# Kernel optimization log

Measured on AMD Instinct MI355X. Metric: run time of the kernel, lower is better.

The kernel has to match this reference:

```python
import jax, jax.numpy as jnp
import numpy as np

B, L, D, V, M = 8, 64, 256, 4096, 16


def _norm(a):
    # torch .std(-1) uses ddof=1 (unbiased)
    return a / (1e-5 + jnp.std(a, axis=-1, keepdims=True, ddof=1))


def setup_inputs() -> dict:
    key = jax.random.key(0)
    ks = jax.random.split(key, 13)
    s = 0.05
    return {
        "x": jax.random.randint(ks[0], (B, L), 0, V),
        "z": jax.random.randint(ks[1], (B, L), 0, V),
        "embed_w": jax.random.normal(ks[2], (V, D), dtype=jnp.float32) * s,
        "init_w": jax.random.normal(ks[3], (D, M), dtype=jnp.float32) * s,
        "trans_w": jax.random.normal(ks[4], (D, D), dtype=jnp.float32) * s,
        "trans_b": jax.random.normal(ks[5], (D,), dtype=jnp.float32) * s,
        "core_w": jax.random.normal(ks[6], (D, D), dtype=jnp.float32) * s,
        "upd_w": jax.random.normal(ks[7], (D, D), dtype=jnp.float32) * s,
        "xks_w": jax.random.normal(ks[8], (2, D), dtype=jnp.float32) * s,
        "xkd_w": jax.random.normal(ks[9], (D, D), dtype=jnp.float32) * s,
        "xkd_b": jax.random.normal(ks[10], (D,), dtype=jnp.float32) * s,
        "emi_w": jax.random.normal(ks[11], (D, D), dtype=jnp.float32) * s,
        "emi_b": jax.random.normal(ks[12], (D,), dtype=jnp.float32) * s,
    }


def reference(x, z, embed_w, init_w, trans_w, trans_b, core_w, upd_w,
              xks_w, xkd_w, xkd_b, emi_w, emi_b):
    # loss() sets y = x * 0 (all-zero token ids)
    ze = _norm(embed_w[z])                      # (B, L, D)
    ye = _norm(embed_w[x * 0])                  # (B, L, D)
    Bq, Lq, Dq = ze.shape

    # init_state.weight.T[None, 0:1] -> column 0, broadcast to (B, L, D), then norm
    xsa0 = _norm(jnp.broadcast_to(init_w[:, 0][None, None, :], (Bq, Lq, Dq)))

    def step(xsa, _):
        xnew = (jnp.roll(xsa, 1, axis=1) @ trans_w
                + jnp.roll(xsa, -1, axis=1) @ trans_w.T
                + xsa @ core_w
                + ze @ upd_w.T
                + trans_b) / 3.0
        return xnew, None

    xsa, _ = jax.lax.scan(step, xsa0, None, length=Lq)

    # mixture head
    xkey_static = jnp.broadcast_to(xks_w[None], (Bq, 2, Dq))          # (B, 2, D)
    xkey_dynamic = ye @ xkd_w.T + xkd_b                                # (B, L, D)
    xkey = jnp.concatenate([xkey_static, xkey_dynamic], axis=1)       # (B, 2+L, D)

    emit = xsa @ emi_w.T + emi_b                                       # (B, L, D)
    cand = jnp.concatenate(
        [emit[:, :, None], ze[:, :, None],
         jnp.broadcast_to(ye[:, None], (Bq, Lq, Lq, Dq))], axis=2)     # (B, L, 2+L, D)

    sel = jax.nn.log_softmax(jnp.einsum('bld,bkd->blk', xsa, xkey), axis=-1)  # (B, L, 2+L)
    lptok_c = jax.nn.log_softmax(cand @ embed_w.T, axis=-1)            # (B, L, 2+L, V)
    lptok = jax.nn.logsumexp(sel[..., None] + lptok_c, axis=-2)        # (B, L, V)
    lptok = jnp.exp(lptok / 2.0)

    cent = jnp.take_along_axis(lptok, x[:, :, None], axis=-1)[..., 0]  # (B, L)
    return -cent.mean(-1)                                              # (B,)
```

## Files before the change

### kernel.cpp

```cpp
#include <hip/hip_runtime.h>
#include <hip/hip_bf16.h>
#include <math.h>

#define BB 8
#define LL 64
#define DD 256
#define VV 4096
#define RR 512
#define K3 768

typedef __attribute__((ext_vector_type(4))) float f32x4;
typedef __attribute__((ext_vector_type(8))) short bf16x8;
typedef __attribute__((ext_vector_type(4))) unsigned short u16x4;
typedef unsigned long long u64;

#define WS_ZE      0
#define WS_ZEU3    (WS_ZE + RR*DD)
#define WS_WCT     (WS_ZEU3 + RR*DD)
#define WS_XSA0    (WS_WCT + DD*K3)
#define WS_XSA1    (WS_XSA0 + RR*DD)
#define WS_EMIT    (WS_XSA1 + RR*DD)
#define WS_YVEC    (WS_EMIT + RR*DD)
#define WS_X0VEC   (WS_YVEC + DD)
#define WS_YK      (WS_X0VEC + DD)
#define WS_YLOG    (WS_YK + DD)
#define WS_YLSE    (WS_YLOG + VV)
#define WS_SEL     (WS_YLSE + 8)
#define WS_TOKS    WS_SEL
#define WS_HPART   WS_WCT
#define WS_TWT     WS_XSA0
#define WS_CWT     (WS_XSA0 + 65536)
#define WS_EHI     861184
#define WS_ELO     (WS_EHI + VV*DD/2)

__device__ __forceinline__ float waveSum(float v) {
#pragma unroll
  for (int o = 32; o > 0; o >>= 1) v += __shfl_xor(v, o, 64);
  return v;
}

__device__ __forceinline__ float blockSum256(float v) {
  __shared__ float red[4];
  int lane = threadIdx.x & 63, w = threadIdx.x >> 6;
  v = waveSum(v);
  __syncthreads();
  if (lane == 0) red[w] = v;
  __syncthreads();
  return red[0] + red[1] + red[2] + red[3];
}

__device__ __forceinline__ unsigned short f2bf(float f) {
  unsigned int u = __float_as_uint(f);
  unsigned int r = (u + 0x7fffu + ((u >> 16) & 1u)) >> 16;
  return (unsigned short)r;
}
__device__ __forceinline__ float bf2f(unsigned short h) {
  return __uint_as_float(((unsigned int)h) << 16);
}

union U64F2 { u64 u; float f[2]; };

__global__ __launch_bounds__(256) void k_norm_rows(
    const int* __restrict__ z, const float* __restrict__ embed,
    const float* __restrict__ initw, float* __restrict__ ws) {
  int r = blockIdx.x, d = threadIdx.x;
  float a; float* dst;
  if (r < RR) { int tok = z[r]; a = embed[tok * DD + d]; dst = ws + WS_ZE + r * DD; }
  else if (r == RR) { a = embed[d]; dst = ws + WS_YVEC; }
  else { a = initw[d * 16]; dst = ws + WS_X0VEC; }
  float s  = blockSum256(a);
  float sq = blockSum256(a * a);
  float mean = s * (1.0f / DD);
  float var = fmaxf((sq - (float)DD * mean * mean) * (1.0f / (DD - 1)), 0.0f);
  dst[d] = a / (1e-5f + sqrtf(var));
}

__global__ __launch_bounds__(256) void k_rowmat2(
    const float* __restrict__ in, const float* __restrict__ W,
    const float* __restrict__ bias, float* __restrict__ out, float scale) {
  int r0 = blockIdx.x * 2, d = threadIdx.x;
  __shared__ float u[2][260];
  u[0][d] = in[r0 * DD + d];
  u[1][d] = in[(r0 + 1) * DD + d];
  __syncthreads();
  float a0 = 0.f, a1 = 0.f;
  const float4* w4 = (const float4*)(W + d * DD);
  const float4* u0 = (const float4*)&u[0][0];
  const float4* u1 = (const float4*)&u[1][0];
#pragma unroll 8
  for (int k4 = 0; k4 < 64; k4++) {
    float4 w = w4[k4], x0 = u0[k4], x1 = u1[k4];
    a0 += x0.x*w.x + x0.y*w.y + x0.z*w.z + x0.w*w.w;
    a1 += x1.x*w.x + x1.y*w.y + x1.z*w.z + x1.w*w.w;
  }
  float b = bias[d];
  out[r0 * DD + d]       = (a0 + b) * scale;
  out[(r0 + 1) * DD + d] = (a1 + b) * scale;
}

__global__ __launch_bounds__(256) void k_tr2(
    const float* __restrict__ tw, const float* __restrict__ cw,
    float* __restrict__ ws) {
  int c = blockIdx.x, k = threadIdx.x;
  ws[WS_TWT + c * DD + k] = tw[k * DD + c];
  ws[WS_CWT + c * DD + k] = cw[k * DD + c];
}

__global__ __launch_bounds__(256) void k_zmat2(
    const float* __restrict__ tw, float* __restrict__ ws) {
  int r0 = blockIdx.x * 2, c = threadIdx.x;
  int b = r0 >> 6, l = r0 & 63;
  const float* zb = ws + WS_ZEU3 + (size_t)b * 64 * DD;
  float* zout = ws + WS_XSA1;
  __shared__ float zs[4][260];
#pragma unroll
  for (int j = 0; j < 4; ++j) {
    int ll = (l + j - 1 + 64) & 63;
    zs[j][c] = zb[ll * DD + c];
  }
  __syncthreads();
  const float4* wA = (const float4*)(ws + WS_TWT + (size_t)c * DD);
  const float4* wB = (const float4*)(tw + (size_t)c * DD);
  const float4* wC = (const float4*)(ws + WS_CWT + (size_t)c * DD);
  const float4* zm0 = (const float4*)&zs[0][0];
  const float4* z00 = (const float4*)&zs[1][0];
  const float4* zp0 = (const float4*)&zs[2][0];
  const float4* zp1 = (const float4*)&zs[3][0];
  float a0 = 0.f, a1 = 0.f;
#pragma unroll 8
  for (int k4 = 0; k4 < 64; ++k4) {
    float4 A4 = wA[k4], B4 = wB[k4], C4 = wC[k4];
    float4 m0 = zm0[k4], z0 = z00[k4], p0 = zp0[k4], p1 = zp1[k4];
    a0 += m0.x*A4.x + m0.y*A4.y + m0.z*A4.z + m0.w*A4.w
        + p0.x*B4.x + p0.y*B4.y + p0.z*B4.z + p0.w*B4.w
        + z0.x*C4.x + z0.y*C4.y + z0.z*C4.z + z0.w*C4.w;
    a1 += z0.x*A4.x + z0.y*A4.y + z0.z*A4.z + z0.w*A4.w
        + p1.x*B4.x + p1.y*B4.y + p1.z*B4.z + p1.w*B4.w
        + p0.x*C4.x + p0.y*C4.y + p0.z*C4.z + p0.w*C4.w;
  }
  const float inv3 = 1.0f / 3.0f;
  zout[(size_t)r0 * DD + c]       = a0 * inv3 + zs[1][c];
  zout[(size_t)(r0 + 1) * DD + c] = a1 * inv3 + zs[2][c];
}

__global__ __launch_bounds__(256) void k_build_w2(
    const float* __restrict__ tw, const float* __restrict__ cw,
    float* __restrict__ ws) {
  int k = blockIdx.x, c = threadIdx.x;
  const float* twT = ws + WS_TWT;
  __shared__ float rA[DD], rB[DD], rC[DD];
  const float inv9 = 1.0f / 9.0f;
  rA[c] = tw[k * DD + c] * inv9;
  rB[c] = twT[k * DD + c] * inv9;
  rC[c] = cw[k * DD + c] * inv9;
  __syncthreads();
  float a2 = 0.f, m1 = 0.f, m0 = 0.f, m3 = 0.f, b2 = 0.f;
#pragma unroll 4
  for (int j = 0; j < DD; ++j) {
    float Aj = tw[j * DD + c];
    float Bj = twT[j * DD + c];
    float Cj = cw[j * DD + c];
    float ra = rA[j], rb = rB[j], rc = rC[j];
    a2 += ra * Aj;
    m1 += rc * Aj + ra * Cj;
    m0 += rb * Aj + ra * Bj + rc * Cj;
    m3 += rc * Bj + rb * Cj;
    b2 += rb * Bj;
  }
  float* p0 = ws + WS_WCT;
  float* p3 = ws + WS_ZEU3;
  p0[k * DD + c]               = a2;
  p0[65536 + k * DD + c]       = m1;
  p0[2 * 65536 + k * DD + c]   = m0;
  p3[k * DD + c]               = m3;
  p3[65536 + k * DD + c]       = b2;
}

__global__ __launch_bounds__(256) void k_split_e(
    const float* __restrict__ e, unsigned short* __restrict__ eh,
    unsigned short* __restrict__ el) {
  int i = (blockIdx.x * 256 + threadIdx.x) * 4;
  float4 v = *(const float4*)(e + i);
  float f[4] = {v.x, v.y, v.z, v.w};
  u16x4 h, l;
#pragma unroll
  for (int j = 0; j < 4; ++j) {
    unsigned short hb = f2bf(f[j]);
    h[j] = hb;
    l[j] = f2bf(f[j] - bf2f(hb));
  }
  *(u16x4*)(eh + i) = h;
  *(u16x4*)(el + i) = l;
}

__global__ __launch_bounds__(256) void k_ylog(
    const float* __restrict__ embed, float* __restrict__ ws) {
  __shared__ float y[DD];
  int t = threadIdx.x;
  y[t] = ws[WS_YVEC + t];
  __syncthreads();
  int w = t >> 6, lane = t & 63;
  for (int i = 0; i < 16; i++) {
    int v = blockIdx.x * 64 + i * 4 + w;
    float p = 0.f;
#pragma unroll
    for (int j = 0; j < 4; j++) p += y[lane + 64*j] * embed[v * DD + lane + 64*j];
    p = waveSum(p);
    if (lane == 0) ws[WS_YLOG + v] = p;
  }
}

__global__ void k_zero_cnt(int* __restrict__ c) {
  c[blockIdx.x * 256 + threadIdx.x] = 0;
}

__global__ __launch_bounds__(256, 2) void k_scan(float* __restrict__ ws) {
  const int bid = blockIdx.x;
  const int rg = bid & 63, cg = bid >> 6;
  const int b = rg >> 3, rgl = rg & 7, l0 = rgl * 8;
  const int t = threadIdx.x, lane = t & 63;
  const int cl = t & 7, rs = t >> 3;
  const int c0 = cg * 32 + cl * 4;

  __shared__ float S[12 * 264];
  __shared__ float PAR[32 * 260];
  __shared__ float PAR2[4 * 256];
  __shared__ float ZB[256];

  int* tok = (int*)(ws + WS_TOKS);

  const float* Wp[5] = {ws + WS_WCT, ws + WS_WCT + 65536, ws + WS_WCT + 2*65536,
                        ws + WS_ZEU3, ws + WS_ZEU3 + 65536};
  f32x4 wreg[40];
#pragma unroll
  for (int p = 0; p < 5; ++p)
#pragma unroll
    for (int q = 0; q < 2; ++q)
#pragma unroll
      for (int kk = 0; kk < 4; ++kk)
        wreg[p * 8 + q * 4 + kk] =
            *(const f32x4*)&Wp[p][(size_t)(rs * 8 + q * 4 + kk) * DD + c0];

  {
    int r = t >> 5, c = t & 31;
    ZB[r * 32 + c] = ws[WS_XSA1 + (size_t)(b * 64 + l0 + r) * DD + cg * 32 + c];
  }

  const int nb0 = b * 8 + ((rgl + 7) & 7);
  const int nb1 = b * 8 + rgl;
  const int nb2 = b * 8 + ((rgl + 1) & 7);
  const int myl = (lane == 0) ? nb0 : (lane == 1) ? nb1 : nb2;

  for (int st = 0; st < 32; ++st) {
    const float* xin  = ws + ((st & 1) ? WS_XSA1 : WS_XSA0);
    float*       xout = ws + ((st & 1) ? WS_XSA0 : WS_XSA1);

    if (st > 0) {
      const int tg = st << 3;
      while (true) {
        int v = __hip_atomic_load(tok + myl * 32, __ATOMIC_RELAXED,
                                  __HIP_MEMORY_SCOPE_AGENT);
        if (__all(v >= tg)) break;
        __builtin_amdgcn_s_sleep(1);
      }
    }

#pragma unroll
    for (int it = 0; it < 6; ++it) {
      int idx = it * 256 + t;
      int j = idx >> 7;
      int kk = (idx & 127) << 1;
      const u64* src = (st == 0)
          ? (const u64*)(ws + WS_X0VEC + kk)
          : (const u64*)(xin + (size_t)(b * 64 + ((l0 + j - 2 + 64) & 63)) * DD + kk);
      u64 v = __hip_atomic_load(src, __ATOMIC_RELAXED, __HIP_MEMORY_SCOPE_AGENT);
      *(u64*)(&S[j * 264 + kk]) = v;
    }
    __syncthreads();

    f32x4 acc[8];
#pragma unroll
    for (int r = 0; r < 8; ++r) acc[r] = (f32x4){0.f, 0.f, 0.f, 0.f};

#pragma unroll
    for (int p = 0; p < 5; ++p) {
#pragma unroll
      for (int r = 0; r < 8; ++r) {
        int j = r + p;
#pragma unroll
        for (int q = 0; q < 2; ++q) {
          f32x4 xv = *(const f32x4*)&S[j * 264 + rs * 8 + q * 4];
          acc[r] += xv.x * wreg[p * 8 + q * 4 + 0];
          acc[r] += xv.y * wreg[p * 8 + q * 4 + 1];
          acc[r] += xv.z * wreg[p * 8 + q * 4 + 2];
          acc[r] += xv.w * wreg[p * 8 + q * 4 + 3];
        }
      }
    }

#pragma unroll
    for (int r = 0; r < 8; ++r)
      *(f32x4*)&PAR[rs * 260 + r * 32 + cl * 4] = acc[r];
    __syncthreads();

    {
      int u = t & 63, v = t >> 6;
      f32x4 s4 = (f32x4){0.f, 0.f, 0.f, 0.f};
#pragma unroll
      for (int i = 0; i < 8; ++i)
        s4 += *(const f32x4*)&PAR[(v * 8 + i) * 260 + u * 4];
      *(f32x4*)&PAR2[v * 256 + u * 4] = s4;
    }
    __syncthreads();

    if (t < 64) {
      int r = t >> 3, c8 = t & 7;
      f32x4 s4 = (f32x4){0.f, 0.f, 0.f, 0.f};
#pragma unroll
      for (int v = 0; v < 4; ++v)
        s4 += *(const f32x4*)&PAR2[v * 256 + t * 4];
      f32x4 zb = *(const f32x4*)&ZB[r * 32 + c8 * 4];
      s4 += zb;
      size_t off = (size_t)(b * 64 + l0 + r) * DD + cg * 32 + c8 * 4;
      U64F2 lo, hi;
      lo.f[0] = s4.x; lo.f[1] = s4.y;
      hi.f[0] = s4.z; hi.f[1] = s4.w;
      __hip_atomic_store((u64*)(xout + off),     lo.u, __ATOMIC_RELAXED, __HIP_MEMORY_SCOPE_AGENT);
      __hip_atomic_store((u64*)(xout + off + 2), hi.u, __ATOMIC_RELAXED, __HIP_MEMORY_SCOPE_AGENT);
    }

    __syncthreads();
    if (t == 0)
      __hip_atomic_fetch_add(tok + nb1 * 32, 1, __ATOMIC_RELAXED,
                             __HIP_MEMORY_SCOPE_AGENT);
  }
}

__global__ __launch_bounds__(256) void k_head_mfma(
    const float* __restrict__ uemit, const float* __restrict__ uze,
    const unsigned short* __restrict__ eh, const unsigned short* __restrict__ el,
    float* __restrict__ hpart) {
  int row0 = blockIdx.x * 32;
  int v0 = blockIdx.y * 128;
  int t = threadIdx.x, lane = t & 63, w = t >> 6;
  int wr = w >> 1, wc = w & 1;
  __shared__ unsigned short UH[32 * 264];
  __shared__ unsigned short UL[32 * 264];
  const float* src = (row0 < RR) ? (uemit + (size_t)row0 * DD)
                                 : (uze + (size_t)(row0 - RR) * DD);
#pragma unroll
  for (int it = 0; it < 4; ++it) {
    int r = it * 8 + (t >> 5);
    int c8 = (t & 31) * 8;
    float4 a = *(const float4*)(src + (size_t)r * DD + c8);
    float4 b2 = *(const float4*)(src + (size_t)r * DD + c8 + 4);
    float fa[8] = {a.x, a.y, a.z, a.w, b2.x, b2.y, b2.z, b2.w};
    u16x4 h0, l0v, h1, l1;
#pragma unroll
    for (int j = 0; j < 4; ++j) {
      unsigned short hb = f2bf(fa[j]);
      h0[j] = hb; l0v[j] = f2bf(fa[j] - bf2f(hb));
      unsigned short hb1 = f2bf(fa[4 + j]);
      h1[j] = hb1; l1[j] = f2bf(fa[4 + j] - bf2f(hb1));
    }
    *(u16x4*)(&UH[r * 264 + c8])     = h0;
    *(u16x4*)(&UH[r * 264 + c8 + 4]) = h1;
    *(u16x4*)(&UL[r * 264 + c8])     = l0v;
    *(u16x4*)(&UL[r * 264 + c8 + 4]) = l1;
  }
  __syncthreads();

  f32x4 acc[4];
#pragma unroll
  for (int q = 0; q < 4; ++q) acc[q] = (f32x4){0.f, 0.f, 0.f, 0.f};

  int arow = wr * 16 + (lane & 15);
  int kof = 8 * (lane >> 4);
  const unsigned short* Ah = &UH[arow * 264 + kof];
  const unsigned short* Al = &UL[arow * 264 + kof];
  int vbase = v0 + wc * 64 + (lane & 15);

#pragma unroll
  for (int p = 0; p < 3; ++p) {
    const unsigned short* Ab = (p == 2) ? Al : Ah;
    const unsigned short* Ebl = ((p == 1) ? el : eh) + (size_t)vbase * DD + kof;
#pragma unroll
    for (int ks = 0; ks < 8; ++ks) {
      int k0 = ks * 32;
      bf16x8 a = *(const bf16x8*)(Ab + k0);
#pragma unroll
      for (int vt = 0; vt < 4; ++vt) {
        bf16x8 bfr = *(const bf16x8*)(Ebl + vt * 16 * DD + k0);
        acc[vt] = __builtin_amdgcn_mfma_f32_16x16x32_bf16(a, bfr, acc[vt], 0, 0, 0);
      }
    }
  }

  int chunk = blockIdx.y * 2 + wc;
#pragma unroll
  for (int i = 0; i < 4; ++i) {
    float mm = -1e30f;
#pragma unroll
    for (int vt = 0; vt < 4; ++vt) mm = fmaxf(mm, acc[vt][i]);
#pragma unroll
    for (int o = 1; o < 16; o <<= 1) mm = fmaxf(mm, __shfl_xor(mm, o, 64));
    float ss = 0.f;
#pragma unroll
    for (int vt = 0; vt < 4; ++vt) ss += __expf(acc[vt][i] - mm);
#pragma unroll
    for (int o = 1; o < 16; o <<= 1) ss += __shfl_xor(ss, o, 64);
    if ((lane & 15) == 0) {
      int row = row0 + wr * 16 + (lane >> 4) * 4 + i;
      hpart[(row * 64 + chunk) * 2]     = mm;
      hpart[(row * 64 + chunk) * 2 + 1] = ss;
    }
  }
}

__global__ __launch_bounds__(256) void k_finish(
    const int* __restrict__ x, const float* __restrict__ embed,
    const float* __restrict__ xks, const float* __restrict__ xkdw,
    const float* __restrict__ xkdb, float* __restrict__ ws,
    float* __restrict__ out) {
  int b = blockIdx.x, t = threadIdx.x, lane = t & 63, w = t >> 6;
  __shared__ float YK[DD];
  __shared__ float rm[4], rv[4];
  __shared__ float ylse_s;
  __shared__ float sel0[64], sel1[64], sel2[64], tg0[64], tg1[64];
  __shared__ float ls0s[64], ls1s[64];

  {
    float acc = xkdb[t];
    const float4* yv4 = (const float4*)(ws + WS_YVEC);
    const float4* w4 = (const float4*)(xkdw + (size_t)t * DD);
    float a = 0.f;
#pragma unroll 8
    for (int k4 = 0; k4 < 64; ++k4) {
      float4 yv = yv4[k4], wv = w4[k4];
      a += yv.x*wv.x + yv.y*wv.y + yv.z*wv.z + yv.w*wv.w;
    }
    YK[t] = acc + a;
  }
  {
    float m = -1e30f, s = 0.f;
    for (int v = t; v < VV; v += 256) {
      float lg = ws[WS_YLOG + v];
      float mn = fmaxf(m, lg);
      s = s * __expf(m - mn) + __expf(lg - mn);
      m = mn;
    }
#pragma unroll
    for (int o = 32; o > 0; o >>= 1) {
      float mo = __shfl_xor(m, o, 64), so = __shfl_xor(s, o, 64);
      float mn = fmaxf(m, mo);
      s = s * __expf(m - mn) + so * __expf(mo - mn);
      m = mn;
    }
    if (lane == 0) { rm[w] = m; rv[w] = s; }
  }
  __syncthreads();
  if (t == 0) {
    float M = fmaxf(fmaxf(rm[0], rm[1]), fmaxf(rm[2], rm[3]));
    float S = rv[0]*__expf(rm[0]-M) + rv[1]*__expf(rm[1]-M) +
              rv[2]*__expf(rm[2]-M) + rv[3]*__expf(rm[3]-M);
    ylse_s = M + logf(S);
  }

  const float* hp = ws + WS_HPART;
  for (int i = 0; i < 16; ++i) {
    int l = w * 16 + i, r = b * 64 + l;
    float4 xs = *(const float4*)&ws[WS_XSA0 + (size_t)r * DD + lane * 4];
    float4 k0 = *(const float4*)&xks[lane * 4];
    float4 k1 = *(const float4*)&xks[DD + lane * 4];
    float4 yk4 = *(const float4*)&YK[lane * 4];
    float s0 = waveSum(xs.x*k0.x + xs.y*k0.y + xs.z*k0.z + xs.w*k0.w);
    float s1 = waveSum(xs.x*k1.x + xs.y*k1.y + xs.z*k1.z + xs.w*k1.w);
    float s2 = waveSum(xs.x*yk4.x + xs.y*yk4.y + xs.z*yk4.z + xs.w*yk4.w);
    int xv = x[r];
    float4 e4 = *(const float4*)&embed[(size_t)xv * DD + lane * 4];
    float4 em = *(const float4*)&ws[WS_EMIT + (size_t)r * DD + lane * 4];
    float4 zr = *(const float4*)&ws[WS_ZE + (size_t)r * DD + lane * 4];
    float t0 = waveSum(em.x*e4.x + em.y*e4.y + em.z*e4.z + em.w*e4.w);
    float t1 = waveSum(zr.x*e4.x + zr.y*e4.y + zr.z*e4.z + zr.w*e4.w);
    float m0 = hp[((size_t)r * 64 + lane) * 2];
    float q0 = hp[((size_t)r * 64 + lane) * 2 + 1];
    float m1 = hp[((size_t)(RR + r) * 64 + lane) * 2];
    float q1 = hp[((size_t)(RR + r) * 64 + lane) * 2 + 1];
#pragma unroll
    for (int o = 32; o > 0; o >>= 1) {
      float mo = __shfl_xor(m0, o, 64), so = __shfl_xor(q0, o, 64);
      float mn = fmaxf(m0, mo);
      q0 = q0 * __expf(m0 - mn) + so * __expf(mo - mn);
      m0 = mn;
      mo = __shfl_xor(m1, o, 64); so = __shfl_xor(q1, o, 64);
      mn = fmaxf(m1, mo);
      q1 = q1 * __expf(m1 - mn) + so * __expf(mo - mn);
      m1 = mn;
    }
    if (lane == 0) {
      sel0[l] = s0; sel1[l] = s1; sel2[l] = s2;
      tg0[l] = t0; tg1[l] = t1;
      ls0s[l] = m0 + logf(q0);
      ls1s[l] = m1 + logf(q1);
    }
  }
  __syncthreads();
  if (w == 0) {
    int l = lane, r = b * 64 + l;
    float s0 = sel0[l], s1 = sel1[l], s2 = sel2[l];
    float mx = fmaxf(s0, fmaxf(s1, s2));
    float den = expf(s0 - mx) + expf(s1 - mx) + 64.f * expf(s2 - mx);
    float lsel = mx + logf(den);
    int xv = x[r];
    float P0 = expf(s0 - lsel + tg0[l] - ls0s[l]);
    float P1 = expf(s1 - lsel + tg1[l] - ls1s[l]);
    float Py = expf(s2 - lsel + ws[WS_YLOG + xv] - ylse_s);
    float cent = sqrtf(P0 + P1 + 64.f * Py);
    float sum = waveSum(cent);
    if (lane == 0) out[b] = -(sum * (1.0f / 64.f));
  }
}

extern "C" void kernel_launch(void* const* d_in, const int* in_sizes, int n_in,
                              void* d_out, int out_size, void* d_ws, size_t ws_size,
                              hipStream_t stream) {
  (void)in_sizes; (void)n_in; (void)out_size; (void)ws_size;
  const int*   x     = (const int*)d_in[0];
  const int*   z     = (const int*)d_in[1];
  const float* embed = (const float*)d_in[2];
  const float* initw = (const float*)d_in[3];
  const float* tw    = (const float*)d_in[4];
  const float* tb    = (const float*)d_in[5];
  const float* cw    = (const float*)d_in[6];
  const float* uw    = (const float*)d_in[7];
  const float* xks   = (const float*)d_in[8];
  const float* xkdw  = (const float*)d_in[9];
  const float* xkdb  = (const float*)d_in[10];
  const float* emiw  = (const float*)d_in[11];
  const float* emib  = (const float*)d_in[12];
  float* ws  = (float*)d_ws;
  float* out = (float*)d_out;

  hipLaunchKernelGGL(k_norm_rows, dim3(RR + 2), dim3(256), 0, stream, z, embed, initw, ws);
  hipLaunchKernelGGL(k_rowmat2,   dim3(256),    dim3(256), 0, stream,
                     ws + WS_ZE, uw, tb, ws + WS_ZEU3, 1.0f / 3.0f);
  hipLaunchKernelGGL(k_tr2,       dim3(256),    dim3(256), 0, stream, tw, cw, ws);
  hipLaunchKernelGGL(k_zmat2,     dim3(256),    dim3(256), 0, stream, tw, ws);
  hipLaunchKernelGGL(k_build_w2,  dim3(256),    dim3(256), 0, stream, tw, cw, ws);
  hipLaunchKernelGGL(k_split_e,   dim3(1024),   dim3(256), 0, stream, embed,
                     (unsigned short*)(ws + WS_EHI), (unsigned short*)(ws + WS_ELO));
  hipLaunchKernelGGL(k_ylog,      dim3(64),     dim3(256), 0, stream, embed, ws);

  hipLaunchKernelGGL(k_zero_cnt, dim3(8), dim3(256), 0, stream, (int*)(ws + WS_TOKS));
  hipLaunchKernelGGL(k_scan, dim3(512), dim3(256), 0, stream, ws);

  hipLaunchKernelGGL(k_rowmat2, dim3(256), dim3(256), 0, stream,
                     ws + WS_XSA0, emiw, emib, ws + WS_EMIT, 1.0f);
  hipLaunchKernelGGL(k_head_mfma, dim3(32, 32), dim3(256), 0, stream,
                     ws + WS_EMIT, ws + WS_ZE,
                     (const unsigned short*)(ws + WS_EHI),
                     (const unsigned short*)(ws + WS_ELO),
                     ws + WS_HPART);
  hipLaunchKernelGGL(k_finish, dim3(8), dim3(256), 0, stream,
                     x, embed, xks, xkdw, xkdb, ws, out);
}
```

Measured before the change: 368.0 us.

## Merge prep kernels and fold embed split, ylog and emit matmul into scan

Folds the ten small launches into four. The transpose goes into the norm kernel, zmat and build_w run as one grid with the counter reset added, and the bf16 embed split, ylog and emit projection are appended to the scan kernel as extra blocks or an epilogue. The aim is to cut launch overhead and let independent work fill idle CUs while the persistent scan runs. The risk is that extra blocks in the scan grid could be scheduled ahead of scan blocks that spin-wait, and the added epilogue wait lengthens the scan blocks.

```diff
diff --git a/kernel.cpp b/kernel.cpp
--- a/kernel.cpp
+++ b/kernel.cpp
@@ -39,16 +39,6 @@
   return v;
 }
 
-__device__ __forceinline__ float blockSum256(float v) {
-  __shared__ float red[4];
-  int lane = threadIdx.x & 63, w = threadIdx.x >> 6;
-  v = waveSum(v);
-  __syncthreads();
-  if (lane == 0) red[w] = v;
-  __syncthreads();
-  return red[0] + red[1] + red[2] + red[3];
-}
-
 __device__ __forceinline__ unsigned short f2bf(float f) {
   unsigned int u = __float_as_uint(f);
   unsigned int r = (u + 0x7fffu + ((u >> 16) & 1u)) >> 16;
@@ -60,19 +50,36 @@
 
 union U64F2 { u64 u; float f[2]; };
 
-__global__ __launch_bounds__(256) void k_norm_rows(
+__global__ __launch_bounds__(256) void k_prep1(
     const int* __restrict__ z, const float* __restrict__ embed,
-    const float* __restrict__ initw, float* __restrict__ ws) {
-  int r = blockIdx.x, d = threadIdx.x;
-  float a; float* dst;
-  if (r < RR) { int tok = z[r]; a = embed[tok * DD + d]; dst = ws + WS_ZE + r * DD; }
-  else if (r == RR) { a = embed[d]; dst = ws + WS_YVEC; }
-  else { a = initw[d * 16]; dst = ws + WS_X0VEC; }
-  float s  = blockSum256(a);
-  float sq = blockSum256(a * a);
-  float mean = s * (1.0f / DD);
-  float var = fmaxf((sq - (float)DD * mean * mean) * (1.0f / (DD - 1)), 0.0f);
-  dst[d] = a / (1e-5f + sqrtf(var));
+    const float* __restrict__ initw, const float* __restrict__ tw,
+    const float* __restrict__ cw, float* __restrict__ ws) {
+  int bid = blockIdx.x, d = threadIdx.x;
+  __shared__ float red[4];
+  if (bid < RR + 2) {
+    float a; float* dst;
+    if (bid < RR) { int tok = z[bid]; a = embed[tok * DD + d]; dst = ws + WS_ZE + bid * DD; }
+    else if (bid == RR) { a = embed[d]; dst = ws + WS_YVEC; }
+    else { a = initw[d * 16]; dst = ws + WS_X0VEC; }
+    int lane = d & 63, w = d >> 6;
+    float s = waveSum(a);
+    __syncthreads();
+    if (lane == 0) red[w] = s;
+    __syncthreads();
+    float sum = red[0] + red[1] + red[2] + red[3];
+    float sq = waveSum(a * a);
+    __syncthreads();
+    if (lane == 0) red[w] = sq;
+    __syncthreads();
+    float sqs = red[0] + red[1] + red[2] + red[3];
+    float mean = sum * (1.0f / DD);
+    float var = fmaxf((sqs - (float)DD * mean * mean) * (1.0f / (DD - 1)), 0.0f);
+    dst[d] = a / (1e-5f + sqrtf(var));
+  } else {
+    int c = bid - (RR + 2);
+    ws[WS_TWT + c * DD + d] = tw[d * DD + c];
+    ws[WS_CWT + c * DD + d] = cw[d * DD + c];
+  }
 }
 
 __global__ __launch_bounds__(256) void k_rowmat2(
@@ -98,134 +105,129 @@
   out[(r0 + 1) * DD + d] = (a1 + b) * scale;
 }
 
-__global__ __launch_bounds__(256) void k_tr2(
+__global__ __launch_bounds__(256) void k_prep3(
     const float* __restrict__ tw, const float* __restrict__ cw,
     float* __restrict__ ws) {
-  int c = blockIdx.x, k = threadIdx.x;
-  ws[WS_TWT + c * DD + k] = tw[k * DD + c];
-  ws[WS_CWT + c * DD + k] = cw[k * DD + c];
-}
-
-__global__ __launch_bounds__(256) void k_zmat2(
-    const float* __restrict__ tw, float* __restrict__ ws) {
-  int r0 = blockIdx.x * 2, c = threadIdx.x;
-  int b = r0 >> 6, l = r0 & 63;
-  const float* zb = ws + WS_ZEU3 + (size_t)b * 64 * DD;
-  float* zout = ws + WS_XSA1;
+  int bid = blockIdx.x, c = threadIdx.x;
   __shared__ float zs[4][260];
-#pragma unroll
-  for (int j = 0; j < 4; ++j) {
-    int ll = (l + j - 1 + 64) & 63;
-    zs[j][c] = zb[ll * DD + c];
-  }
-  __syncthreads();
-  const float4* wA = (const float4*)(ws + WS_TWT + (size_t)c * DD);
-  const float4* wB = (const float4*)(tw + (size_t)c * DD);
-  const float4* wC = (const float4*)(ws + WS_CWT + (size_t)c * DD);
-  const float4* zm0 = (const float4*)&zs[0][0];
-  const float4* z00 = (const float4*)&zs[1][0];
-  const float4* zp0 = (const float4*)&zs[2][0];
-  const float4* zp1 = (const float4*)&zs[3][0];
-  float a0 = 0.f, a1 = 0.f;
+  __shared__ float rA[DD], rB[DD], rC[DD];
+  if (bid < 256) {
+    int r0 = bid * 2;
+    int b = r0 >> 6, l = r0 & 63;
+    const float* zb = ws + WS_ZEU3 + (size_t)b * 64 * DD;
+    float* zout = ws + WS_XSA1;
+#pragma unroll
+    for (int j = 0; j < 4; ++j) {
+      int ll = (l + j - 1 + 64) & 63;
+      zs[j][c] = zb[ll * DD + c];
+    }
+    __syncthreads();
+    const float4* wA = (const float4*)(ws + WS_TWT + (size_t)c * DD);
+    const float4* wB = (const float4*)(tw + (size_t)c * DD);
+    const float4* wC = (const float4*)(ws + WS_CWT + (size_t)c * DD);
+    const float4* zm0 = (const float4*)&zs[0][0];
+    const float4* z00 = (const float4*)&zs[1][0];
+    const float4* zp0 = (const float4*)&zs[2][0];
+    const float4* zp1 = (const float4*)&zs[3][0];
+    float a0 = 0.f, a1 = 0.f;
 #pragma unroll 8
-  for (int k4 = 0; k4 < 64; ++k4) {
-    float4 A4 = wA[k4], B4 = wB[k4], C4 = wC[k4];
-    float4 m0 = zm0[k4], z0 = z00[k4], p0 = zp0[k4], p1 = zp1[k4];
-    a0 += m0.x*A4.x + m0.y*A4.y + m0.z*A4.z + m0.w*A4.w
-        + p0.x*B4.x + p0.y*B4.y + p0.z*B4.z + p0.w*B4.w
-        + z0.x*C4.x + z0.y*C4.y + z0.z*C4.z + z0.w*C4.w;
-    a1 += z0.x*A4.x + z0.y*A4.y + z0.z*A4.z + z0.w*A4.w
-        + p1.x*B4.x + p1.y*B4.y + p1.z*B4.z + p1.w*B4.w
-        + p0.x*C4.x + p0.y*C4.y + p0.z*C4.z + p0.w*C4.w;
-  }
-  const float inv3 = 1.0f / 3.0f;
-  zout[(size_t)r0 * DD + c]       = a0 * inv3 + zs[1][c];
-  zout[(size_t)(r0 + 1) * DD + c] = a1 * inv3 + zs[2][c];
-}
-
-__global__ __launch_bounds__(256) void k_build_w2(
-    const float* __restrict__ tw, const float* __restrict__ cw,
-    float* __restrict__ ws) {
-  int k = blockIdx.x, c = threadIdx.x;
-  const float* twT = ws + WS_TWT;
-  __shared__ float rA[DD], rB[DD], rC[DD];
-  const float inv9 = 1.0f / 9.0f;
-  rA[c] = tw[k * DD + c] * inv9;
-  rB[c] = twT[k * DD + c] * inv9;
-  rC[c] = cw[k * DD + c] * inv9;
-  __syncthreads();
-  float a2 = 0.f, m1 = 0.f, m0 = 0.f, m3 = 0.f, b2 = 0.f;
+    for (int k4 = 0; k4 < 64; ++k4) {
+      float4 A4 = wA[k4], B4 = wB[k4], C4 = wC[k4];
+      float4 m0 = zm0[k4], z0 = z00[k4], p0 = zp0[k4], p1 = zp1[k4];
+      a0 += m0.x*A4.x + m0.y*A4.y + m0.z*A4.z + m0.w*A4.w
+          + p0.x*B4.x + p0.y*B4.y + p0.z*B4.z + p0.w*B4.w
+          + z0.x*C4.x + z0.y*C4.y + z0.z*C4.z + z0.w*C4.w;
+      a1 += z0.x*A4.x + z0.y*A4.y + z0.z*A4.z + z0.w*A4.w
+          + p1.x*B4.x + p1.y*B4.y + p1.z*B4.z + p1.w*B4.w
+          + p0.x*C4.x + p0.y*C4.y + p0.z*C4.z + p0.w*C4.w;
+    }
+    const float inv3 = 1.0f / 3.0f;
+    zout[(size_t)r0 * DD + c]       = a0 * inv3 + zs[1][c];
+    zout[(size_t)(r0 + 1) * DD + c] = a1 * inv3 + zs[2][c];
+  } else if (bid < 512) {
+    int k = bid - 256;
+    const float* twT = ws + WS_TWT;
+    const float inv9 = 1.0f / 9.0f;
+    rA[c] = tw[k * DD + c] * inv9;
+    rB[c] = twT[k * DD + c] * inv9;
+    rC[c] = cw[k * DD + c] * inv9;
+    __syncthreads();
+    float a2 = 0.f, m1 = 0.f, m0 = 0.f, m3 = 0.f, b2 = 0.f;
 #pragma unroll 4
-  for (int j = 0; j < DD; ++j) {
-    float Aj = tw[j * DD + c];
-    float Bj = twT[j * DD + c];
-    float Cj = cw[j * DD + c];
-    float ra = rA[j], rb = rB[j], rc = rC[j];
-    a2 += ra * Aj;
-    m1 += rc * Aj + ra * Cj;
-    m0 += rb * Aj + ra * Bj + rc * Cj;
-    m3 += rc * Bj + rb * Cj;
-    b2 += rb * Bj;
-  }
-  float* p0 = ws + WS_WCT;
-  float* p3 = ws + WS_ZEU3;
-  p0[k * DD + c]               = a2;
-  p0[65536 + k * DD + c]       = m1;
-  p0[2 * 65536 + k * DD + c]   = m0;
-  p3[k * DD + c]               = m3;
-  p3[65536 + k * DD + c]       = b2;
-}
-
-__global__ __launch_bounds__(256) void k_split_e(
-    const float* __restrict__ e, unsigned short* __restrict__ eh,
-    unsigned short* __restrict__ el) {
-  int i = (blockIdx.x * 256 + threadIdx.x) * 4;
-  float4 v = *(const float4*)(e + i);
-  float f[4] = {v.x, v.y, v.z, v.w};
-  u16x4 h, l;
-#pragma unroll
-  for (int j = 0; j < 4; ++j) {
-    unsigned short hb = f2bf(f[j]);
-    h[j] = hb;
-    l[j] = f2bf(f[j] - bf2f(hb));
-  }
-  *(u16x4*)(eh + i) = h;
-  *(u16x4*)(el + i) = l;
-}
-
-__global__ __launch_bounds__(256) void k_ylog(
-    const float* __restrict__ embed, float* __restrict__ ws) {
-  __shared__ float y[DD];
-  int t = threadIdx.x;
-  y[t] = ws[WS_YVEC + t];
-  __syncthreads();
-  int w = t >> 6, lane = t & 63;
-  for (int i = 0; i < 16; i++) {
-    int v = blockIdx.x * 64 + i * 4 + w;
-    float p = 0.f;
-#pragma unroll
-    for (int j = 0; j < 4; j++) p += y[lane + 64*j] * embed[v * DD + lane + 64*j];
-    p = waveSum(p);
-    if (lane == 0) ws[WS_YLOG + v] = p;
-  }
-}
-
-__global__ void k_zero_cnt(int* __restrict__ c) {
-  c[blockIdx.x * 256 + threadIdx.x] = 0;
-}
-
-__global__ __launch_bounds__(256, 2) void k_scan(float* __restrict__ ws) {
+    for (int j = 0; j < DD; ++j) {
+      float Aj = tw[j * DD + c];
+      float Bj = twT[j * DD + c];
+      float Cj = cw[j * DD + c];
+      float ra = rA[j], rb = rB[j], rc = rC[j];
+      a2 += ra * Aj;
+      m1 += rc * Aj + ra * Cj;
+      m0 += rb * Aj + ra * Bj + rc * Cj;
+      m3 += rc * Bj + rb * Cj;
+      b2 += rb * Bj;
+    }
+    float* p0 = ws + WS_WCT;
+    float* p3 = ws + WS_ZEU3;
+    p0[k * DD + c]               = a2;
+    p0[65536 + k * DD + c]       = m1;
+    p0[2 * 65536 + k * DD + c]   = m0;
+    p3[k * DD + c]               = m3;
+    p3[65536 + k * DD + c]       = b2;
+  } else {
+    ((int*)(ws + WS_TOKS))[(bid - 512) * 256 + c] = 0;
+  }
+}
+
+__global__ __launch_bounds__(256, 2) void k_scan_big(
+    float* __restrict__ ws, const float* __restrict__ embed,
+    const float* __restrict__ emiw, const float* __restrict__ emib) {
   const int bid = blockIdx.x;
-  const int rg = bid & 63, cg = bid >> 6;
-  const int b = rg >> 3, rgl = rg & 7, l0 = rgl * 8;
   const int t = threadIdx.x, lane = t & 63;
-  const int cl = t & 7, rs = t >> 3;
-  const int c0 = cg * 32 + cl * 4;
 
   __shared__ float S[12 * 264];
   __shared__ float PAR[32 * 260];
   __shared__ float PAR2[4 * 256];
   __shared__ float ZB[256];
+
+  if (bid >= 512) {
+    int eb = bid - 512;
+    if (eb < 1024) {
+      unsigned short* eh = (unsigned short*)(ws + WS_EHI);
+      unsigned short* el = (unsigned short*)(ws + WS_ELO);
+      int i = (eb * 256 + t) * 4;
+      float4 v = *(const float4*)(embed + i);
+      float f[4] = {v.x, v.y, v.z, v.w};
+      u16x4 h, l;
+#pragma unroll
+      for (int j = 0; j < 4; ++j) {
+        unsigned short hb = f2bf(f[j]);
+        h[j] = hb;
+        l[j] = f2bf(f[j] - bf2f(hb));
+      }
+      *(u16x4*)(eh + i) = h;
+      *(u16x4*)(el + i) = l;
+    } else {
+      int yb = eb - 1024;
+      float* y = S;
+      y[t] = ws[WS_YVEC + t];
+      __syncthreads();
+      int w = t >> 6;
+      for (int i = 0; i < 16; i++) {
+        int v = yb * 64 + i * 4 + w;
+        float p = 0.f;
+#pragma unroll
+        for (int j = 0; j < 4; j++)
+          p += y[lane + 64*j] * embed[(size_t)v * DD + lane + 64*j];
+        p = waveSum(p);
+        if (lane == 0) ws[WS_YLOG + v] = p;
+      }
+    }
+    return;
+  }
+
+  const int rg = bid & 63, cg = bid >> 6;
+  const int b = rg >> 3, rgl = rg & 7, l0 = rgl * 8;
+  const int cl = t & 7, rs = t >> 3;
+  const int c0 = cg * 32 + cl * 4;
 
   int* tok = (int*)(ws + WS_TOKS);
 
@@ -333,6 +335,36 @@
     if (t == 0)
       __hip_atomic_fetch_add(tok + nb1 * 32, 1, __ATOMIC_RELAXED,
                              __HIP_MEMORY_SCOPE_AGENT);
+  }
+
+  if (t == 0) {
+    while (__hip_atomic_load(tok + nb1 * 32, __ATOMIC_RELAXED,
+                             __HIP_MEMORY_SCOPE_AGENT) < 256)
+      __builtin_amdgcn_s_sleep(1);
+  }
+  __syncthreads();
+#pragma unroll
+  for (int it = 0; it < 4; ++it) {
+    int idx = it * 256 + t;
+    int j = idx >> 7;
+    int kk = (idx & 127) << 1;
+    u64 v = __hip_atomic_load(
+        (const u64*)(ws + WS_XSA0 + (size_t)(b * 64 + l0 + j) * DD + kk),
+        __ATOMIC_RELAXED, __HIP_MEMORY_SCOPE_AGENT);
+    *(u64*)(&S[j * 264 + kk]) = v;
+  }
+  __syncthreads();
+  {
+    int r = t >> 5, c = cg * 32 + (t & 31);
+    const float4* wv = (const float4*)(emiw + (size_t)c * DD);
+    const float4* xv = (const float4*)&S[r * 264];
+    float a = 0.f;
+#pragma unroll 8
+    for (int k4 = 0; k4 < 64; ++k4) {
+      float4 w = wv[k4], x = xv[k4];
+      a += x.x*w.x + x.y*w.y + x.z*w.z + x.w*w.w;
+    }
+    ws[WS_EMIT + (size_t)(b * 64 + l0 + r) * DD + c] = a + emib[c];
   }
 }
 
@@ -541,21 +573,13 @@
   float* ws  = (float*)d_ws;
   float* out = (float*)d_out;
 
-  hipLaunchKernelGGL(k_norm_rows, dim3(RR + 2), dim3(256), 0, stream, z, embed, initw, ws);
-  hipLaunchKernelGGL(k_rowmat2,   dim3(256),    dim3(256), 0, stream,
+  hipLaunchKernelGGL(k_prep1, dim3(RR + 2 + 256), dim3(256), 0, stream,
+                     z, embed, initw, tw, cw, ws);
+  hipLaunchKernelGGL(k_rowmat2, dim3(256), dim3(256), 0, stream,
                      ws + WS_ZE, uw, tb, ws + WS_ZEU3, 1.0f / 3.0f);
-  hipLaunchKernelGGL(k_tr2,       dim3(256),    dim3(256), 0, stream, tw, cw, ws);
-  hipLaunchKernelGGL(k_zmat2,     dim3(256),    dim3(256), 0, stream, tw, ws);
-  hipLaunchKernelGGL(k_build_w2,  dim3(256),    dim3(256), 0, stream, tw, cw, ws);
-  hipLaunchKernelGGL(k_split_e,   dim3(1024),   dim3(256), 0, stream, embed,
-                     (unsigned short*)(ws + WS_EHI), (unsigned short*)(ws + WS_ELO));
-  hipLaunchKernelGGL(k_ylog,      dim3(64),     dim3(256), 0, stream, embed, ws);
-
-  hipLaunchKernelGGL(k_zero_cnt, dim3(8), dim3(256), 0, stream, (int*)(ws + WS_TOKS));
-  hipLaunchKernelGGL(k_scan, dim3(512), dim3(256), 0, stream, ws);
-
-  hipLaunchKernelGGL(k_rowmat2, dim3(256), dim3(256), 0, stream,
-                     ws + WS_XSA0, emiw, emib, ws + WS_EMIT, 1.0f);
+  hipLaunchKernelGGL(k_prep3, dim3(520), dim3(256), 0, stream, tw, cw, ws);
+  hipLaunchKernelGGL(k_scan_big, dim3(1600), dim3(256), 0, stream,
+                     ws, embed, emiw, emib);
   hipLaunchKernelGGL(k_head_mfma, dim3(32, 32), dim3(256), 0, stream,
                      ws + WS_EMIT, ws + WS_ZE,
                      (const unsigned short*)(ws + WS_EHI),
```

Result: faster. 353.4 us (-4.0%).
